# Performance work log

Measured on AMD Instinct MI355X. Metric: run time of the kernel, lower is better.

Reference implementation:

```python
import jax, jax.numpy as jnp
import numpy as np

B, S, E, H = 2, 2048, 1024, 16
D = E // H  # head dim = 64


def setup_inputs() -> dict:
    key = jax.random.key(0)
    ks = jax.random.split(key, 8)
    return {
        "query": jax.random.normal(ks[0], (B, S, E), dtype=jnp.float32),
        "key": jax.random.normal(ks[1], (B, S, E), dtype=jnp.float32),
        "value": jax.random.normal(ks[2], (B, S, E), dtype=jnp.float32),
        "qkv_weight": jax.random.normal(ks[3], (3 * E, E), dtype=jnp.float32) * 0.02,
        "qkv_bias": jax.random.normal(ks[4], (3 * E,), dtype=jnp.float32) * 0.02,
        "proj_weight": jax.random.normal(ks[5], (E, E), dtype=jnp.float32) * 0.02,
        "proj_bias": jax.random.normal(ks[6], (E,), dtype=jnp.float32) * 0.02,
        "mask": jax.random.normal(ks[7], (S, S), dtype=jnp.float32),
    }


def reference(query, key, value, qkv_weight, qkv_bias, proj_weight, proj_bias, mask):
    # Split fused QKV weight/bias into per-projection chunks ([E,E] each).
    wq, wk, wv = jnp.split(qkv_weight, 3, axis=0)
    bq, bk, bv = jnp.split(qkv_bias, 3, axis=0)

    def proj_heads(x, w, b):
        # [B,S,E] @ [E,E]^T + [E] -> [B,H,S,D]
        y = jnp.einsum("bse,fe->bsf", x, w) + b
        return y.reshape(B, S, H, D).transpose(0, 2, 1, 3)

    q = proj_heads(query, wq, bq)
    k = proj_heads(key, wk, bk)
    v = proj_heads(value, wv, bv)

    scale = 1.0 / jnp.sqrt(jnp.asarray(D, dtype=q.dtype))
    # scores: [B,H,S,S]; mask_type 0 -> additive [S,S] float mask broadcast over B,H
    scores = jnp.einsum("bhsd,bhtd->bhst", q, k) * scale + mask[None, None, :, :]
    attn = jax.nn.softmax(scores, axis=-1)
    ctx = jnp.einsum("bhst,bhtd->bhsd", attn, v)  # [B,H,S,D]
    ctx = ctx.transpose(0, 2, 1, 3).reshape(B, S, E)
    # output projection
    return jnp.einsum("bse,fe->bsf", ctx, proj_weight) + proj_bias
```

## Files before the change

### kernel.cpp

```cpp
#include <hip/hip_runtime.h>
#include <hip/hip_bf16.h>

typedef unsigned short u16;
typedef __attribute__((ext_vector_type(8))) __bf16 bf16x8;
typedef __attribute__((ext_vector_type(4))) __bf16 bf16x4;
typedef __attribute__((ext_vector_type(4))) float f32x4;
typedef __attribute__((ext_vector_type(16))) float f32x16;

#define LOG2E 1.44269504f

#if __has_builtin(__builtin_amdgcn_exp2f)
#define EXP2F(x) __builtin_amdgcn_exp2f(x)
#else
#define EXP2F(x) __expf((x) * 0.69314718f)
#endif

#define GLL16(gptr, lptr) \
  __builtin_amdgcn_global_load_lds((__attribute__((address_space(1))) void*)(gptr), \
                                   (__attribute__((address_space(3))) void*)(lptr), 16, 0, 0)

static __device__ __forceinline__ u16 f2bf(float f) {
  union { float f; unsigned u; } v; v.f = f;
  unsigned r = (v.u + 0x7FFFu + ((v.u >> 16) & 1u)) >> 16;
  return (u16)r;
}

__global__ __launch_bounds__(256) void cvt_all(
    const float* __restrict__ q, const float* __restrict__ k, const float* __restrict__ v,
    const float* __restrict__ w1, const float* __restrict__ w2,
    u16* __restrict__ xq, u16* __restrict__ xk, u16* __restrict__ xv,
    u16* __restrict__ wq, u16* __restrict__ wp) {
  const int b = blockIdx.x;
  const float* src; u16* dst; int off;
  if (b < 4096)       { src = q;  dst = xq; off = b; }
  else if (b < 8192)  { src = k;  dst = xk; off = b - 4096; }
  else if (b < 12288) { src = v;  dst = xv; off = b - 8192; }
  else if (b < 15360) { src = w1; dst = wq; off = b - 12288; }
  else                { src = w2; dst = wp; off = b - 15360; }
  const int i = off * 256 + threadIdx.x;
  float4 vv = ((const float4*)src)[i];
  ushort4 o;
  o.x = f2bf(vv.x); o.y = f2bf(vv.y); o.z = f2bf(vv.z); o.w = f2bf(vv.w);
  ((ushort4*)dst)[i] = o;
}

__global__ __launch_bounds__(256, 2) void qkv_gemm(
    const u16* __restrict__ xq, const u16* __restrict__ xk, const u16* __restrict__ xv,
    const u16* __restrict__ wbf, const float* __restrict__ bias,
    u16* __restrict__ qout, u16* __restrict__ kout, u16* __restrict__ vtout) {
  __shared__ u16 Al[128 * 32];
  __shared__ u16 Bl[128 * 32];
  const int tid = threadIdx.x;
  const int lane = tid & 63;
  const int w = tid >> 6;
  const int wr = w >> 1, wc = w & 1;
  const int nb = blockIdx.x, mb = blockIdx.y;
  const int row0 = mb * 128;
  const int ncol0 = nb * 128;
  const int which = nb >> 3;
  const u16* A = (which == 0) ? xq : (which == 1) ? xk : xv;
  const u16* Bw = wbf + (size_t)ncol0 * 1024;

  f32x4 acc[4][4];
  f32x4 zero = {0.f, 0.f, 0.f, 0.f};
#pragma unroll
  for (int i = 0; i < 4; i++)
#pragma unroll
    for (int j = 0; j < 4; j++) acc[i][j] = zero;

  const int srow = w * 16 + (lane >> 2);
  const int scol = (lane & 3) * 8;

  for (int k0 = 0; k0 < 1024; k0 += 32) {
#pragma unroll
    for (int p = 0; p < 2; p++) {
      const u16* ga = A + (size_t)(row0 + p * 64 + srow) * 1024 + k0 + scol;
      GLL16(ga, &Al[(p * 64 + w * 16) * 32]);
      const u16* gb = Bw + (size_t)(p * 64 + srow) * 1024 + k0 + scol;
      GLL16(gb, &Bl[(p * 64 + w * 16) * 32]);
    }
    __syncthreads();
    bf16x8 af[4], bfr[4];
#pragma unroll
    for (int mi = 0; mi < 4; mi++)
      af[mi] = *(const bf16x8*)&Al[(wr * 64 + mi * 16 + (lane & 15)) * 32 + (lane >> 4) * 8];
#pragma unroll
    for (int ni = 0; ni < 4; ni++)
      bfr[ni] = *(const bf16x8*)&Bl[(wc * 64 + ni * 16 + (lane & 15)) * 32 + (lane >> 4) * 8];
#pragma unroll
    for (int mi = 0; mi < 4; mi++)
#pragma unroll
      for (int ni = 0; ni < 4; ni++)
        acc[mi][ni] = __builtin_amdgcn_mfma_f32_16x16x32_bf16(af[mi], bfr[ni], acc[mi][ni], 0, 0, 0);
    __syncthreads();
  }

#pragma unroll
  for (int mi = 0; mi < 4; mi++) {
    const int rb = row0 + wr * 64 + mi * 16 + (lane >> 4) * 4;
#pragma unroll
    for (int ni = 0; ni < 4; ni++) {
      const int c = ncol0 + wc * 64 + ni * 16 + (lane & 15);
      const float bs = bias[c];
      const float sc = (which == 0) ? (0.125f * LOG2E) : 1.0f;
      const int fm = c & 1023;
      const int h = fm >> 6, d = fm & 63;
#pragma unroll
      for (int r = 0; r < 4; r++) {
        const int rr = rb + r;
        const int b = rr >> 11, s = rr & 2047;
        const u16 val = f2bf((acc[mi][ni][r] + bs) * sc);
        if (which == 0)
          qout[(((size_t)(b * 16 + h)) * 2048 + s) * 64 + d] = val;
        else if (which == 1)
          kout[(((size_t)(b * 16 + h)) * 2048 + s) * 64 + d] = val;
        else
          vtout[(((size_t)(b * 16 + h)) * 64 + d) * 2048 + s] = val;
      }
    }
  }
}


#define MFMA32(A, B, C) __builtin_amdgcn_mfma_f32_32x32x16_bf16(A, B, C, 0, 0, 0)

#define TILE_BODY(KOFF, MA, MB)                                                    \
  {                                                                                \
    f32x16 sA, sB;                                                                 \
    __builtin_amdgcn_s_setprio(1);                                                 \
    {                                                                              \
      const char* kb0 = ldsb + (KOFF) + Kb;                                        \
      sA = MFMA32(*(const bf16x8*)(kb0 + o0), qf0, MA);                            \
      sB = MFMA32(*(const bf16x8*)(kb0 + 4096 + o0), qf0, MB);                     \
      sA = MFMA32(*(const bf16x8*)(kb0 + o1), qf1, sA);                            \
      sB = MFMA32(*(const bf16x8*)(kb0 + 4096 + o1), qf1, sB);                     \
      sA = MFMA32(*(const bf16x8*)(kb0 + o2), qf2, sA);                            \
      sB = MFMA32(*(const bf16x8*)(kb0 + 4096 + o2), qf2, sB);                     \
      sA = MFMA32(*(const bf16x8*)(kb0 + o3), qf3, sA);                            \
      sB = MFMA32(*(const bf16x8*)(kb0 + 4096 + o3), qf3, sB);                     \
    }                                                                              \
    __builtin_amdgcn_s_setprio(0);                                                 \
    float pm = fmaxf(                                                              \
        fmaxf(fmaxf(fmaxf(fmaxf(sA[0], sA[1]), fmaxf(sA[2], sA[3])),               \
                    fmaxf(fmaxf(sA[4], sA[5]), fmaxf(sA[6], sA[7]))),              \
              fmaxf(fmaxf(fmaxf(sA[8], sA[9]), fmaxf(sA[10], sA[11])),             \
                    fmaxf(fmaxf(sA[12], sA[13]), fmaxf(sA[14], sA[15])))),         \
        fmaxf(fmaxf(fmaxf(fmaxf(sB[0], sB[1]), fmaxf(sB[2], sB[3])),               \
                    fmaxf(fmaxf(sB[4], sB[5]), fmaxf(sB[6], sB[7]))),              \
              fmaxf(fmaxf(fmaxf(sB[8], sB[9]), fmaxf(sB[10], sB[11])),             \
                    fmaxf(fmaxf(sB[12], sB[13]), fmaxf(sB[14], sB[15])))));        \
                     \
    _Pragma("unroll")                                                              \
    for (int e_ = 0; e_ < 16; e_++) { sA[e_] = EXP2F(sA[e_] - m); }                \
    _Pragma("unroll")                                                              \
    for (int e_ = 0; e_ < 16; e_++) { sB[e_] = EXP2F(sB[e_] - m); }                \
    float ps = (((sA[0] + sA[1]) + (sA[2] + sA[3])) +                              \
                ((sA[4] + sA[5]) + (sA[6] + sA[7]))) +                             \
               (((sA[8] + sA[9]) + (sA[10] + sA[11])) +                            \
                ((sA[12] + sA[13]) + (sA[14] + sA[15]))) +                         \
               (((sB[0] + sB[1]) + (sB[2] + sB[3])) +                              \
                ((sB[4] + sB[5]) + (sB[6] + sB[7]))) +                             \
               (((sB[8] + sB[9]) + (sB[10] + sB[11])) +                            \
                ((sB[12] + sB[13]) + (sB[14] + sB[15])));                          \
    pm = fmaxf(pm, __shfl_xor(pm, 32));                                            \
    if (__any(pm > m + 8.0f)) {                 \
      const float mn = fmaxf(m, pm);                                               \
      const float al = EXP2F(m - mn);                                              \
      m = mn; lsum *= al; ps *= al;                                                \
      sA *= al; sB *= al; ctx0 *= al; ctx1 *= al;                                  \
    }                                                                              \
    lsum += ps;                                                                    \
    bf16x8 pa0, pa1, pa2, pa3;                                                     \
    _Pragma("unroll")                                                              \
    for (int e_ = 0; e_ < 8; e_++) {                                               \
      pa0[e_] = (__bf16)sA[e_]; pa1[e_] = (__bf16)sA[8 + e_];                      \
      pa2[e_] = (__bf16)sB[e_]; pa3[e_] = (__bf16)sB[8 + e_];                      \
    }                                                                              \
    {                                                                              \
      const char* vb0 = ldsb + 16384 + (KOFF) + Vb;                                \
      __builtin_amdgcn_s_setprio(1);                                               \
      ctx0 = MFMA32(*(const bf16x8*)(vb0 + 0), pa0, ctx0);                         \
      ctx1 = MFMA32(*(const bf16x8*)(vb0 + 1024), pa0, ctx1);                      \
      ctx0 = MFMA32(*(const bf16x8*)(vb0 + 2048), pa1, ctx0);                      \
      ctx1 = MFMA32(*(const bf16x8*)(vb0 + 3072), pa1, ctx1);                      \
      ctx0 = MFMA32(*(const bf16x8*)(vb0 + 4096), pa2, ctx0);                      \
      ctx1 = MFMA32(*(const bf16x8*)(vb0 + 5120), pa2, ctx1);                      \
      ctx0 = MFMA32(*(const bf16x8*)(vb0 + 6144), pa3, ctx0);                      \
      ctx1 = MFMA32(*(const bf16x8*)(vb0 + 7168), pa3, ctx1);                      \
      __builtin_amdgcn_s_setprio(0);                                               \
    }                                                                              \
  }

__global__ __launch_bounds__(256, 2) void attn_fwd(
    const u16* __restrict__ qbf, const u16* __restrict__ kbf, const u16* __restrict__ vtbf,
    const float* __restrict__ mask, u16* __restrict__ ctxout) {
  __shared__ u16 lds[16384];
  char* ldsb = (char*)lds;
  const int tid = threadIdx.x, lane = tid & 63, w = tid >> 6;
  const int q32 = lane & 31, hi = lane >> 5;
  const int bh = blockIdx.x, qt = blockIdx.y;
  const int qbase = qt * 128;
  const size_t hbase = (size_t)bh * 2048 * 64;
  const int qglob = qbase + w * 32 + q32;

  const int x = (q32 & 7) << 4;
  const int Kb = q32 * 128;
  const int o0 = (0 + hi * 16) ^ x;
  const int o1 = (32 + hi * 16) ^ x;
  const int o2 = (64 + hi * 16) ^ x;
  const int o3 = (96 + hi * 16) ^ x;
  const int Vb = hi * 512 + q32 * 16;
  const int srow = tid >> 3, Ac = tid & 7;
  const int S0 = srow * 128 + ((Ac * 16) ^ ((srow & 7) << 4));
  const int S1 = S0 + 4096;
  const int jv = Ac >> 1, epos = (Ac & 1) * 8;
  const int VW0 = jv * 2048 + srow * 16 + epos;
  const int VW1 = jv * 2048 + 1024 + srow * 16 + epos;

  const u16* qrow = qbf + hbase + (size_t)qglob * 64 + hi * 8;
  bf16x8 qf0 = *(const bf16x8*)(qrow + 0);
  bf16x8 qf1 = *(const bf16x8*)(qrow + 16);
  bf16x8 qf2 = *(const bf16x8*)(qrow + 32);
  bf16x8 qf3 = *(const bf16x8*)(qrow + 48);

  float4 kr0, kr1, vr0, vr1;
  kr0 = *(const float4*)&kbf[hbase + (size_t)srow * 64 + Ac * 8];
  kr1 = *(const float4*)&kbf[hbase + (size_t)(32 + srow) * 64 + Ac * 8];
  vr0 = *(const float4*)&vtbf[hbase + (size_t)srow * 2048 + Ac * 8];
  vr1 = *(const float4*)&vtbf[hbase + (size_t)(32 + srow) * 2048 + Ac * 8];
  *(float4*)(ldsb + S0) = kr0;
  *(float4*)(ldsb + S1) = kr1;
  *(float2*)(ldsb + 16384 + VW0) = make_float2(vr0.x, vr0.y);
  *(float2*)(ldsb + 16384 + VW0 + 512) = make_float2(vr0.z, vr0.w);
  *(float2*)(ldsb + 16384 + VW1) = make_float2(vr1.x, vr1.y);
  *(float2*)(ldsb + 16384 + VW1 + 512) = make_float2(vr1.z, vr1.w);
  kr0 = *(const float4*)&kbf[hbase + (size_t)(64 + srow) * 64 + Ac * 8];
  kr1 = *(const float4*)&kbf[hbase + (size_t)(96 + srow) * 64 + Ac * 8];
  vr0 = *(const float4*)&vtbf[hbase + (size_t)srow * 2048 + 64 + Ac * 8];
  vr1 = *(const float4*)&vtbf[hbase + (size_t)(32 + srow) * 2048 + 64 + Ac * 8];

  const u16* kp = kbf + hbase + (size_t)(128 + srow) * 64 + Ac * 8;
  const u16* vp = vtbf + hbase + (size_t)srow * 2048 + 128 + Ac * 8;
  const float* mpp = mask + (size_t)qglob * 2048 + hi * 4;

  f32x16 mcA, mcB, mdA, mdB;
#pragma unroll
  for (int jq = 0; jq < 4; jq++) {
    ((f32x4*)&mcA)[jq] = (*(const f32x4*)(mpp + jq * 8)) * LOG2E;
    ((f32x4*)&mcB)[jq] = (*(const f32x4*)(mpp + 32 + jq * 8)) * LOG2E;
  }

  float m = 0.f, lsum = 0.f;
  f32x16 ctx0 = (f32x16)(0.f), ctx1 = (f32x16)(0.f);

  __syncthreads();

  for (int i = 0; i < 16; ++i) {
    *(float4*)(ldsb + 8192 + S0) = kr0;
    *(float4*)(ldsb + 8192 + S1) = kr1;
    *(float2*)(ldsb + 24576 + VW0) = make_float2(vr0.x, vr0.y);
    *(float2*)(ldsb + 24576 + VW0 + 512) = make_float2(vr0.z, vr0.w);
    *(float2*)(ldsb + 24576 + VW1) = make_float2(vr1.x, vr1.y);
    *(float2*)(ldsb + 24576 + VW1 + 512) = make_float2(vr1.z, vr1.w);
    if (i < 15) {
      kr0 = *(const float4*)kp;
      kr1 = *(const float4*)(kp + 2048);
      vr0 = *(const float4*)vp;
      vr1 = *(const float4*)(vp + 65536);
      kp += 4096; vp += 64;
    }
#pragma unroll
    for (int jq = 0; jq < 4; jq++) {
      ((f32x4*)&mdA)[jq] = (*(const f32x4*)(mpp + 64 + jq * 8)) * LOG2E;
      ((f32x4*)&mdB)[jq] = (*(const f32x4*)(mpp + 96 + jq * 8)) * LOG2E;
    }
    TILE_BODY(0, mcA, mcB)
    __syncthreads();

    if (i < 15) {
      *(float4*)(ldsb + S0) = kr0;
      *(float4*)(ldsb + S1) = kr1;
      *(float2*)(ldsb + 16384 + VW0) = make_float2(vr0.x, vr0.y);
      *(float2*)(ldsb + 16384 + VW0 + 512) = make_float2(vr0.z, vr0.w);
      *(float2*)(ldsb + 16384 + VW1) = make_float2(vr1.x, vr1.y);
      *(float2*)(ldsb + 16384 + VW1 + 512) = make_float2(vr1.z, vr1.w);
      kr0 = *(const float4*)kp;
      kr1 = *(const float4*)(kp + 2048);
      vr0 = *(const float4*)vp;
      vr1 = *(const float4*)(vp + 65536);
      kp += 4096; vp += 64;
#pragma unroll
      for (int jq = 0; jq < 4; jq++) {
        ((f32x4*)&mcA)[jq] = (*(const f32x4*)(mpp + 128 + jq * 8)) * LOG2E;
        ((f32x4*)&mcB)[jq] = (*(const f32x4*)(mpp + 160 + jq * 8)) * LOG2E;
      }
    }
    TILE_BODY(8192, mdA, mdB)
    mpp += 128;
    __syncthreads();
  }

  lsum += __shfl_xor(lsum, 32);
  const float inv = 1.0f / lsum;
  const int b = bh >> 4, h = bh & 15;
  u16* orow = ctxout + (size_t)(b * 2048 + qglob) * 1024 + h * 64;
#pragma unroll
  for (int jq = 0; jq < 4; jq++) {
    bf16x4 o0, o1;
#pragma unroll
    for (int rr = 0; rr < 4; rr++) {
      o0[rr] = (__bf16)(ctx0[4 * jq + rr] * inv);
      o1[rr] = (__bf16)(ctx1[4 * jq + rr] * inv);
    }
    *(bf16x4*)&orow[jq * 8 + hi * 4] = o0;
    *(bf16x4*)&orow[32 + jq * 8 + hi * 4] = o1;
  }
}

__global__ __launch_bounds__(256, 2) void proj_gemm(
    const u16* __restrict__ ctx, const u16* __restrict__ wbf,
    const float* __restrict__ bias, float* __restrict__ out) {
  __shared__ u16 Al[128 * 32];
  __shared__ u16 Bl[128 * 32];
  const int tid = threadIdx.x;
  const int lane = tid & 63;
  const int w = tid >> 6;
  const int wr = w >> 1, wc = w & 1;
  const int nb = blockIdx.x, mb = blockIdx.y;
  const int row0 = mb * 128;
  const int ncol0 = nb * 128;
  const u16* Bw = wbf + (size_t)ncol0 * 1024;

  f32x4 acc[4][4];
  f32x4 zero = {0.f, 0.f, 0.f, 0.f};
#pragma unroll
  for (int i = 0; i < 4; i++)
#pragma unroll
    for (int j = 0; j < 4; j++) acc[i][j] = zero;

  const int srow = w * 16 + (lane >> 2);
  const int scol = (lane & 3) * 8;

  for (int k0 = 0; k0 < 1024; k0 += 32) {
#pragma unroll
    for (int p = 0; p < 2; p++) {
      const u16* ga = ctx + (size_t)(row0 + p * 64 + srow) * 1024 + k0 + scol;
      GLL16(ga, &Al[(p * 64 + w * 16) * 32]);
      const u16* gb = Bw + (size_t)(p * 64 + srow) * 1024 + k0 + scol;
      GLL16(gb, &Bl[(p * 64 + w * 16) * 32]);
    }
    __syncthreads();
    bf16x8 af[4], bfr[4];
#pragma unroll
    for (int mi = 0; mi < 4; mi++)
      af[mi] = *(const bf16x8*)&Al[(wr * 64 + mi * 16 + (lane & 15)) * 32 + (lane >> 4) * 8];
#pragma unroll
    for (int ni = 0; ni < 4; ni++)
      bfr[ni] = *(const bf16x8*)&Bl[(wc * 64 + ni * 16 + (lane & 15)) * 32 + (lane >> 4) * 8];
#pragma unroll
    for (int mi = 0; mi < 4; mi++)
#pragma unroll
      for (int ni = 0; ni < 4; ni++)
        acc[mi][ni] = __builtin_amdgcn_mfma_f32_16x16x32_bf16(af[mi], bfr[ni], acc[mi][ni], 0, 0, 0);
    __syncthreads();
  }

#pragma unroll
  for (int mi = 0; mi < 4; mi++) {
    const int rb = row0 + wr * 64 + mi * 16 + (lane >> 4) * 4;
#pragma unroll
    for (int ni = 0; ni < 4; ni++) {
      const int c = ncol0 + wc * 64 + ni * 16 + (lane & 15);
      const float bs = bias[c];
#pragma unroll
      for (int r = 0; r < 4; r++)
        out[(size_t)(rb + r) * 1024 + c] = acc[mi][ni][r] + bs;
    }
  }
}

extern "C" void kernel_launch(void* const* d_in, const int* in_sizes, int n_in,
                              void* d_out, int out_size, void* d_ws, size_t ws_size,
                              hipStream_t stream) {
  const float* query = (const float*)d_in[0];
  const float* key   = (const float*)d_in[1];
  const float* value = (const float*)d_in[2];
  const float* qkvw  = (const float*)d_in[3];
  const float* qkvb  = (const float*)d_in[4];
  const float* projw = (const float*)d_in[5];
  const float* projb = (const float*)d_in[6];
  const float* mask  = (const float*)d_in[7];

  char* ws = (char*)d_ws;
  u16* xq    = (u16*)(ws + 0);
  u16* xk    = (u16*)(ws + 8388608);
  u16* xv    = (u16*)(ws + 16777216);
  u16* wqkv  = (u16*)(ws + 25165824);
  u16* wproj = (u16*)(ws + 31457280);
  u16* qb    = (u16*)(ws + 33554432);
  u16* kb    = (u16*)(ws + 41943040);
  u16* vt    = (u16*)(ws + 50331648);
  u16* cx    = xq;

  cvt_all<<<16384, 256, 0, stream>>>(query, key, value, qkvw, projw, xq, xk, xv, wqkv, wproj);
  qkv_gemm<<<dim3(24, 32), 256, 0, stream>>>(xq, xk, xv, wqkv, qkvb, qb, kb, vt);
  attn_fwd<<<dim3(32, 16), 256, 0, stream>>>(qb, kb, vt, mask, cx);
  proj_gemm<<<dim3(8, 32), 256, 0, stream>>>(cx, wproj, projb, (float*)d_out);
}
```

Before: 169.2 us.

## Split attention KV range across two wave groups and merge partial softmax states

The attention kernel now runs 512 threads per block, with two halves of four waves each handling half of the key/value sequence for the same 128 queries (split-K flash attention). Each half keeps its own online max/sum and context, and at the end the second half writes its state to LDS so the first half can rescale and merge before writing output. LDS doubles to 64KB and the V tile layout gains an XOR swizzle on both stores and reads to reduce bank conflicts. This shortens the serial KV loop per wave and raises wave count per CU, at the cost of a final merge step, more LDS, and possible occupancy limits.

```diff
diff --git a/kernel.cpp b/kernel.cpp
--- a/kernel.cpp
+++ b/kernel.cpp
@@ -129,7 +129,7 @@
     f32x16 sA, sB;                                                                 \
     __builtin_amdgcn_s_setprio(1);                                                 \
     {                                                                              \
-      const char* kb0 = ldsb + (KOFF) + Kb;                                        \
+      const char* kb0 = ldsb + hbK + (KOFF) + Kb;                                  \
       sA = MFMA32(*(const bf16x8*)(kb0 + o0), qf0, MA);                            \
       sB = MFMA32(*(const bf16x8*)(kb0 + 4096 + o0), qf0, MB);                     \
       sA = MFMA32(*(const bf16x8*)(kb0 + o1), qf1, sA);                            \
@@ -149,7 +149,6 @@
                     fmaxf(fmaxf(sB[4], sB[5]), fmaxf(sB[6], sB[7]))),              \
               fmaxf(fmaxf(fmaxf(sB[8], sB[9]), fmaxf(sB[10], sB[11])),             \
                     fmaxf(fmaxf(sB[12], sB[13]), fmaxf(sB[14], sB[15])))));        \
-                     \
     _Pragma("unroll")                                                              \
     for (int e_ = 0; e_ < 16; e_++) { sA[e_] = EXP2F(sA[e_] - m); }                \
     _Pragma("unroll")                                                              \
@@ -177,31 +176,48 @@
       pa2[e_] = (__bf16)sB[e_]; pa3[e_] = (__bf16)sB[8 + e_];                      \
     }                                                                              \
     {                                                                              \
-      const char* vb0 = ldsb + 16384 + (KOFF) + Vb;                                \
+      const char* vb0 = ldsb + hbV + (KOFF);                                       \
       __builtin_amdgcn_s_setprio(1);                                               \
-      ctx0 = MFMA32(*(const bf16x8*)(vb0 + 0), pa0, ctx0);                         \
-      ctx1 = MFMA32(*(const bf16x8*)(vb0 + 1024), pa0, ctx1);                      \
-      ctx0 = MFMA32(*(const bf16x8*)(vb0 + 2048), pa1, ctx0);                      \
-      ctx1 = MFMA32(*(const bf16x8*)(vb0 + 3072), pa1, ctx1);                      \
-      ctx0 = MFMA32(*(const bf16x8*)(vb0 + 4096), pa2, ctx0);                      \
-      ctx1 = MFMA32(*(const bf16x8*)(vb0 + 5120), pa2, ctx1);                      \
-      ctx0 = MFMA32(*(const bf16x8*)(vb0 + 6144), pa3, ctx0);                      \
-      ctx1 = MFMA32(*(const bf16x8*)(vb0 + 7168), pa3, ctx1);                      \
+      ctx0 = MFMA32(*(const bf16x8*)(vb0 + Vr0), pa0, ctx0);                       \
+      ctx1 = MFMA32(*(const bf16x8*)(vb0 + Vr1), pa0, ctx1);                       \
+      ctx0 = MFMA32(*(const bf16x8*)(vb0 + Vr2), pa1, ctx0);                       \
+      ctx1 = MFMA32(*(const bf16x8*)(vb0 + Vr3), pa1, ctx1);                       \
+      ctx0 = MFMA32(*(const bf16x8*)(vb0 + Vr4), pa2, ctx0);                       \
+      ctx1 = MFMA32(*(const bf16x8*)(vb0 + Vr5), pa2, ctx1);                       \
+      ctx0 = MFMA32(*(const bf16x8*)(vb0 + Vr6), pa3, ctx0);                       \
+      ctx1 = MFMA32(*(const bf16x8*)(vb0 + Vr7), pa3, ctx1);                       \
       __builtin_amdgcn_s_setprio(0);                                               \
     }                                                                              \
   }
 
-__global__ __launch_bounds__(256, 2) void attn_fwd(
+#define STAGE_KV(KOFF)                                                             \
+  {                                                                                \
+    char* ks = ldsb + hbK + (KOFF);                                                \
+    char* vs = ldsb + hbV + (KOFF);                                                \
+    *(float4*)(ks + S0) = kr0;                                                     \
+    *(float4*)(ks + S0 + 4096) = kr1;                                              \
+    *(float2*)(vs + VWa) = make_float2(vr0.x, vr0.y);                              \
+    *(float2*)(vs + VWa + 512) = make_float2(vr0.z, vr0.w);                        \
+    *(float2*)(vs + VWc) = make_float2(vr1.x, vr1.y);                              \
+    *(float2*)(vs + VWc + 512) = make_float2(vr1.z, vr1.w);                        \
+  }
+
+__global__ __launch_bounds__(512, 4) void attn_fwd(
     const u16* __restrict__ qbf, const u16* __restrict__ kbf, const u16* __restrict__ vtbf,
     const float* __restrict__ mask, u16* __restrict__ ctxout) {
-  __shared__ u16 lds[16384];
+  __shared__ u16 lds[32768];
   char* ldsb = (char*)lds;
   const int tid = threadIdx.x, lane = tid & 63, w = tid >> 6;
   const int q32 = lane & 31, hi = lane >> 5;
+  const int hb = w >> 2;
+  const int w4 = w & 3;
+  const int th = hb << 10;
+  const int hbK = hb * 16384;
+  const int hbV = 32768 + hb * 16384;
   const int bh = blockIdx.x, qt = blockIdx.y;
   const int qbase = qt * 128;
   const size_t hbase = (size_t)bh * 2048 * 64;
-  const int qglob = qbase + w * 32 + q32;
+  const int qglob = qbase + w4 * 32 + q32;
 
   const int x = (q32 & 7) << 4;
   const int Kb = q32 * 128;
@@ -209,13 +225,21 @@
   const int o1 = (32 + hi * 16) ^ x;
   const int o2 = (64 + hi * 16) ^ x;
   const int o3 = (96 + hi * 16) ^ x;
-  const int Vb = hi * 512 + q32 * 16;
-  const int srow = tid >> 3, Ac = tid & 7;
+  const int vbr = hi * 512 + q32 * 16;
+  const int Vr0 = 0 * 1024 + (vbr ^ 0);
+  const int Vr1 = 1 * 1024 + (vbr ^ 16);
+  const int Vr2 = 2 * 1024 + (vbr ^ 32);
+  const int Vr3 = 3 * 1024 + (vbr ^ 48);
+  const int Vr4 = 4 * 1024 + (vbr ^ 64);
+  const int Vr5 = 5 * 1024 + (vbr ^ 80);
+  const int Vr6 = 6 * 1024 + (vbr ^ 96);
+  const int Vr7 = 7 * 1024 + (vbr ^ 112);
+  const int srow = (tid >> 3) & 31, Ac = tid & 7;
   const int S0 = srow * 128 + ((Ac * 16) ^ ((srow & 7) << 4));
-  const int S1 = S0 + 4096;
   const int jv = Ac >> 1, epos = (Ac & 1) * 8;
-  const int VW0 = jv * 2048 + srow * 16 + epos;
-  const int VW1 = jv * 2048 + 1024 + srow * 16 + epos;
+  const int cA = 2 * jv, cB = 2 * jv + 1;
+  const int VWa = cA * 1024 + ((srow * 16) ^ (cA << 4)) + epos;
+  const int VWc = cB * 1024 + ((srow * 16) ^ (cB << 4)) + epos;
 
   const u16* qrow = qbf + hbase + (size_t)qglob * 64 + hi * 8;
   bf16x8 qf0 = *(const bf16x8*)(qrow + 0);
@@ -224,24 +248,19 @@
   bf16x8 qf3 = *(const bf16x8*)(qrow + 48);
 
   float4 kr0, kr1, vr0, vr1;
-  kr0 = *(const float4*)&kbf[hbase + (size_t)srow * 64 + Ac * 8];
-  kr1 = *(const float4*)&kbf[hbase + (size_t)(32 + srow) * 64 + Ac * 8];
-  vr0 = *(const float4*)&vtbf[hbase + (size_t)srow * 2048 + Ac * 8];
-  vr1 = *(const float4*)&vtbf[hbase + (size_t)(32 + srow) * 2048 + Ac * 8];
-  *(float4*)(ldsb + S0) = kr0;
-  *(float4*)(ldsb + S1) = kr1;
-  *(float2*)(ldsb + 16384 + VW0) = make_float2(vr0.x, vr0.y);
-  *(float2*)(ldsb + 16384 + VW0 + 512) = make_float2(vr0.z, vr0.w);
-  *(float2*)(ldsb + 16384 + VW1) = make_float2(vr1.x, vr1.y);
-  *(float2*)(ldsb + 16384 + VW1 + 512) = make_float2(vr1.z, vr1.w);
-  kr0 = *(const float4*)&kbf[hbase + (size_t)(64 + srow) * 64 + Ac * 8];
-  kr1 = *(const float4*)&kbf[hbase + (size_t)(96 + srow) * 64 + Ac * 8];
-  vr0 = *(const float4*)&vtbf[hbase + (size_t)srow * 2048 + 64 + Ac * 8];
-  vr1 = *(const float4*)&vtbf[hbase + (size_t)(32 + srow) * 2048 + 64 + Ac * 8];
-
-  const u16* kp = kbf + hbase + (size_t)(128 + srow) * 64 + Ac * 8;
-  const u16* vp = vtbf + hbase + (size_t)srow * 2048 + 128 + Ac * 8;
-  const float* mpp = mask + (size_t)qglob * 2048 + hi * 4;
+  kr0 = *(const float4*)&kbf[hbase + (size_t)(th + srow) * 64 + Ac * 8];
+  kr1 = *(const float4*)&kbf[hbase + (size_t)(th + 32 + srow) * 64 + Ac * 8];
+  vr0 = *(const float4*)&vtbf[hbase + (size_t)srow * 2048 + th + Ac * 8];
+  vr1 = *(const float4*)&vtbf[hbase + (size_t)(32 + srow) * 2048 + th + Ac * 8];
+  STAGE_KV(0)
+  kr0 = *(const float4*)&kbf[hbase + (size_t)(th + 64 + srow) * 64 + Ac * 8];
+  kr1 = *(const float4*)&kbf[hbase + (size_t)(th + 96 + srow) * 64 + Ac * 8];
+  vr0 = *(const float4*)&vtbf[hbase + (size_t)srow * 2048 + th + 64 + Ac * 8];
+  vr1 = *(const float4*)&vtbf[hbase + (size_t)(32 + srow) * 2048 + th + 64 + Ac * 8];
+
+  const u16* kp = kbf + hbase + (size_t)(th + 128 + srow) * 64 + Ac * 8;
+  const u16* vp = vtbf + hbase + (size_t)srow * 2048 + th + 128 + Ac * 8;
+  const float* mpp = mask + (size_t)qglob * 2048 + th + hi * 4;
 
   f32x16 mcA, mcB, mdA, mdB;
 #pragma unroll
@@ -255,14 +274,9 @@
 
   __syncthreads();
 
-  for (int i = 0; i < 16; ++i) {
-    *(float4*)(ldsb + 8192 + S0) = kr0;
-    *(float4*)(ldsb + 8192 + S1) = kr1;
-    *(float2*)(ldsb + 24576 + VW0) = make_float2(vr0.x, vr0.y);
-    *(float2*)(ldsb + 24576 + VW0 + 512) = make_float2(vr0.z, vr0.w);
-    *(float2*)(ldsb + 24576 + VW1) = make_float2(vr1.x, vr1.y);
-    *(float2*)(ldsb + 24576 + VW1 + 512) = make_float2(vr1.z, vr1.w);
-    if (i < 15) {
+  for (int j = 0; j < 8; ++j) {
+    STAGE_KV(8192)
+    if (j < 7) {
       kr0 = *(const float4*)kp;
       kr1 = *(const float4*)(kp + 2048);
       vr0 = *(const float4*)vp;
@@ -277,13 +291,8 @@
     TILE_BODY(0, mcA, mcB)
     __syncthreads();
 
-    if (i < 15) {
-      *(float4*)(ldsb + S0) = kr0;
-      *(float4*)(ldsb + S1) = kr1;
-      *(float2*)(ldsb + 16384 + VW0) = make_float2(vr0.x, vr0.y);
-      *(float2*)(ldsb + 16384 + VW0 + 512) = make_float2(vr0.z, vr0.w);
-      *(float2*)(ldsb + 16384 + VW1) = make_float2(vr1.x, vr1.y);
-      *(float2*)(ldsb + 16384 + VW1 + 512) = make_float2(vr1.z, vr1.w);
+    if (j < 7) {
+      STAGE_KV(0)
       kr0 = *(const float4*)kp;
       kr1 = *(const float4*)(kp + 2048);
       vr0 = *(const float4*)vp;
@@ -300,20 +309,38 @@
     __syncthreads();
   }
 
-  lsum += __shfl_xor(lsum, 32);
-  const float inv = 1.0f / lsum;
-  const int b = bh >> 4, h = bh & 15;
-  u16* orow = ctxout + (size_t)(b * 2048 + qglob) * 1024 + h * 64;
-#pragma unroll
-  for (int jq = 0; jq < 4; jq++) {
-    bf16x4 o0, o1;
-#pragma unroll
-    for (int rr = 0; rr < 4; rr++) {
-      o0[rr] = (__bf16)(ctx0[4 * jq + rr] * inv);
-      o1[rr] = (__bf16)(ctx1[4 * jq + rr] * inv);
-    }
-    *(bf16x4*)&orow[jq * 8 + hi * 4] = o0;
-    *(bf16x4*)&orow[32 + jq * 8 + hi * 4] = o1;
+  if (w >= 4) {
+    char* cw = ldsb + (w - 4) * 9216 + lane * 144;
+    *(f32x16*)cw = ctx0;
+    *(f32x16*)(cw + 64) = ctx1;
+    ((float*)cw)[32] = m;
+    ((float*)cw)[33] = lsum;
+  }
+  __syncthreads();
+  if (w < 4) {
+    const char* cw = ldsb + w * 9216 + lane * 144;
+    f32x16 cb0 = *(const f32x16*)cw;
+    f32x16 cb1 = *(const f32x16*)(cw + 64);
+    const float mb = ((const float*)cw)[32];
+    const float lb = ((const float*)cw)[33];
+    const float mm = fmaxf(m, mb);
+    const float fa = EXP2F(m - mm), fb = EXP2F(mb - mm);
+    lsum = lsum * fa + lb * fb;
+    lsum += __shfl_xor(lsum, 32);
+    const float inv = 1.0f / lsum;
+    const int b = bh >> 4, h = bh & 15;
+    u16* orow = ctxout + (size_t)(b * 2048 + qglob) * 1024 + h * 64;
+#pragma unroll
+    for (int jq = 0; jq < 4; jq++) {
+      bf16x4 oA, oB;
+#pragma unroll
+      for (int rr = 0; rr < 4; rr++) {
+        oA[rr] = (__bf16)((ctx0[4 * jq + rr] * fa + cb0[4 * jq + rr] * fb) * inv);
+        oB[rr] = (__bf16)((ctx1[4 * jq + rr] * fa + cb1[4 * jq + rr] * fb) * inv);
+      }
+      *(bf16x4*)&orow[jq * 8 + hi * 4] = oA;
+      *(bf16x4*)&orow[32 + jq * 8 + hi * 4] = oB;
+    }
   }
 }
 
@@ -404,6 +431,6 @@
 
   cvt_all<<<16384, 256, 0, stream>>>(query, key, value, qkvw, projw, xq, xk, xv, wqkv, wproj);
   qkv_gemm<<<dim3(24, 32), 256, 0, stream>>>(xq, xk, xv, wqkv, qkvb, qb, kb, vt);
-  attn_fwd<<<dim3(32, 16), 256, 0, stream>>>(qb, kb, vt, mask, cx);
+  attn_fwd<<<dim3(32, 16), 512, 0, stream>>>(qb, kb, vt, mask, cx);
   proj_gemm<<<dim3(8, 32), 256, 0, stream>>>(cx, wproj, projb, (float*)d_out);
 }
```

New measurement: 370.2 us. +118.8%, slower.
